# Kernel optimization log

Hardware: AMD Instinct MI355X
Metric: run time of the kernel (lower is better)

## Reference

```python
import jax, jax.numpy as jnp
import numpy as np

H, KV, Dh = 16, 4, 128
ROPE_BASE = 10000.0


def _rope(x, pos):
    # x: (B, nh, T, Dh); pos: (T,)
    inv = 1.0 / (ROPE_BASE ** (jnp.arange(0, Dh, 2, dtype=jnp.float32) / Dh))  # (Dh/2,)
    freqs = pos.astype(jnp.float32)[:, None] * inv[None, :]                    # (T, Dh/2)
    cos = jnp.cos(freqs).astype(x.dtype)[None, None]                           # (1,1,T,Dh/2)
    sin = jnp.sin(freqs).astype(x.dtype)[None, None]
    x1, x2 = x[..., ::2], x[..., 1::2]
    o1 = x1 * cos - x2 * sin
    o2 = x1 * sin + x2 * cos
    return jnp.stack([o1, o2], axis=-1).reshape(x.shape)


def setup_inputs() -> dict:
    key = jax.random.key(0)
    ks = jax.random.split(key, 5)
    B, T, d = 2, 2048, 2048
    s = 1.0 / np.sqrt(d)
    return {
        "x": jax.random.normal(ks[0], (B, T, d), dtype=jnp.float32),
        "Wq": jax.random.normal(ks[1], (d, H * Dh), dtype=jnp.float32) * s,
        "Wk": jax.random.normal(ks[2], (d, KV * Dh), dtype=jnp.float32) * s,
        "Wv": jax.random.normal(ks[3], (d, KV * Dh), dtype=jnp.float32) * s,
        "Wo": jax.random.normal(ks[4], (H * Dh, d), dtype=jnp.float32) * s,
    }


def reference(x, Wq, Wk, Wv, Wo):
    B, T, d = x.shape
    rep = H // KV
    q = (x @ Wq).reshape(B, T, H, Dh).transpose(0, 2, 1, 3)   # (B,H,T,Dh)
    k = (x @ Wk).reshape(B, T, KV, Dh).transpose(0, 2, 1, 3)  # (B,KV,T,Dh)
    v = (x @ Wv).reshape(B, T, KV, Dh).transpose(0, 2, 1, 3)

    pos = jnp.arange(T)
    q = _rope(q, pos)
    k = _rope(k, pos)

    # GQA repeat_kv: (B,KV,T,Dh) -> (B,H,T,Dh), heads repeated consecutively
    k_full = jnp.repeat(k, rep, axis=1)
    v_full = jnp.repeat(v, rep, axis=1)

    scale = 1.0 / np.sqrt(Dh)
    scores = jnp.einsum('bhqd,bhkd->bhqk', q, k_full) * scale  # (B,H,T,T)
    causal = jnp.tril(jnp.ones((T, T), dtype=bool))
    scores = jnp.where(causal[None, None], scores, -jnp.inf)
    attn = jax.nn.softmax(scores, axis=-1)
    out = jnp.einsum('bhqk,bhkd->bhqd', attn, v_full)          # (B,H,T,Dh)
    out = out.transpose(0, 2, 1, 3).reshape(B, T, H * Dh)
    return out @ Wo
```

## Files before the change

### kernel.cpp

```cpp
#include <hip/hip_runtime.h>
#include <stdint.h>

typedef __bf16 bf16;
typedef __bf16 bf16x8 __attribute__((ext_vector_type(8)));
typedef __bf16 bf16x4 __attribute__((ext_vector_type(4)));
typedef float  f32x4  __attribute__((ext_vector_type(4)));

#define T_SEQ  2048
#define NHEAD  16
#define DHEAD  128
#define DMODEL 2048
#define NQKV   3072
#define UNROLL _Pragma("unroll")

__device__ __forceinline__ void gload_lds16(const void* g, void* l) {
  __builtin_amdgcn_global_load_lds(
      (const __attribute__((address_space(1))) uint32_t*)g,
      (__attribute__((address_space(3))) uint32_t*)l, 16, 0, 0);
}

__device__ __forceinline__ void twt_body(const float* __restrict__ W,
                                         bf16* __restrict__ WT, int K, int N,
                                         int bx, int by, float (*t)[65]) {
  int k0 = bx * 64, n0 = by * 64;
  int r4 = threadIdx.x >> 6, c = threadIdx.x & 63;
#pragma unroll
  for (int i = 0; i < 16; i++) {
    int r = i * 4 + r4;
    t[r][c] = W[(size_t)(k0 + r) * N + n0 + c];
  }
  __syncthreads();
#pragma unroll
  for (int i = 0; i < 16; i++) {
    int r = i * 4 + r4;
    WT[(size_t)(n0 + r) * K + k0 + c] = (bf16)t[c][r];
  }
}

__global__ __launch_bounds__(256) void k_prep(const float* __restrict__ x,
                                              const float* __restrict__ Wq,
                                              const float* __restrict__ Wk,
                                              const float* __restrict__ Wv,
                                              const float* __restrict__ Wo,
                                              bf16* __restrict__ xb,
                                              bf16* __restrict__ WT,
                                              bf16* __restrict__ WoT) {
  __shared__ float t[64][65];
  const int blk = blockIdx.x;
  if (blk < 8192) {
    int i = (blk * 256 + threadIdx.x) * 4;
    float4 v = *(const float4*)(x + i);
    bf16x4 o = { (bf16)v.x, (bf16)v.y, (bf16)v.z, (bf16)v.w };
    *(bf16x4*)(xb + i) = o;
  } else if (blk < 9216) {
    int b = blk - 8192;
    twt_body(Wq, WT, 2048, 2048, b & 31, b >> 5, t);
  } else if (blk < 9472) {
    int b = blk - 9216;
    twt_body(Wk, WT + (size_t)2048 * 2048, 2048, 512, b & 31, b >> 5, t);
  } else if (blk < 9728) {
    int b = blk - 9472;
    twt_body(Wv, WT + (size_t)2560 * 2048, 2048, 512, b & 31, b >> 5, t);
  } else {
    int b = blk - 9728;
    twt_body(Wo, WoT, 2048, 2048, b & 31, b >> 5, t);
  }
}

__global__ __launch_bounds__(256) void k_post(bf16* __restrict__ QKV,
                                              bf16* __restrict__ Vtg) {
  __shared__ bf16 t[64][65];
  const int blk = blockIdx.x;
  if (blk < 5120) {
    const float L2B = 0.20762050593046007f;
    int tid = blk * 256 + threadIdx.x;
    int row = tid / 320;
    int c8 = (tid - row * 320) * 8;
    int tt = row & (T_SEQ - 1);
    bf16* p = QKV + (size_t)row * NQKV + c8;
    bf16x8 v = *(const bf16x8*)p;
    int ib = (c8 & 127) >> 1;
    bf16x8 o;
#pragma unroll
    for (int m = 0; m < 4; m++) {
      float inv = exp2f(-(float)(ib + m) * L2B);
      float ang = (float)tt * inv;
      float cs, sn;
      __sincosf(ang, &sn, &cs);
      float x1 = (float)v[2 * m], x2 = (float)v[2 * m + 1];
      o[2 * m]     = (bf16)(x1 * cs - x2 * sn);
      o[2 * m + 1] = (bf16)(x1 * sn + x2 * cs);
    }
    *(bf16x8*)p = o;
  } else {
    int bb = blk - 5120;
    int bx = bb & 31, by = (bb >> 5) & 1, g = bb >> 6;
    const int t0 = bx * 64, d0 = by * 64;
    const int b = g >> 2, kvh = g & 3;
    const bf16* src = QKV + (size_t)b * T_SEQ * NQKV + 2560 + kvh * DHEAD;
    bf16* dst = Vtg + ((size_t)(b * 4 + kvh) * 128 + d0) * T_SEQ + t0;
    const int r4 = threadIdx.x >> 6, c = threadIdx.x & 63;
#pragma unroll
    for (int i = 0; i < 16; i++) {
      int r = i * 4 + r4;
      t[r][c] = src[(size_t)(t0 + r) * NQKV + d0 + c];
    }
    __syncthreads();
#pragma unroll
    for (int i = 0; i < 16; i++) {
      int r = i * 4 + r4;
      dst[(size_t)r * T_SEQ + c] = t[c][r];
    }
  }
}

#define PH(BUF, P, RB, VMW, STAGE) do {                                                   \
    bf16x8 a0k0 = rdA(BUF, 2*(P),     0), a0k1 = rdA(BUF, 2*(P),     1);                  \
    bf16x8 a1k0 = rdA(BUF, 2*(P) + 1, 0), a1k1 = rdA(BUF, 2*(P) + 1, 1);                  \
    if (RB) {                                                                             \
      UNROLL for (int n = 0; n < 4; n++) { b0[n] = rdB(BUF, 0, n); b1[n] = rdB(BUF, 1, n); } \
    }                                                                                     \
    STAGE                                                                                 \
    __builtin_amdgcn_sched_barrier(0);                                                    \
    __builtin_amdgcn_s_barrier();                                                         \
    asm volatile("s_waitcnt lgkmcnt(0)" ::: "memory");                                    \
    __builtin_amdgcn_sched_barrier(0);                                                    \
    __builtin_amdgcn_s_setprio(1);                                                        \
    UNROLL for (int n = 0; n < 4; n++) {                                                  \
      acc[2*(P)][n]   = __builtin_amdgcn_mfma_f32_16x16x32_bf16(a0k0, b0[n], acc[2*(P)][n], 0, 0, 0);     \
      acc[2*(P)][n]   = __builtin_amdgcn_mfma_f32_16x16x32_bf16(a0k1, b1[n], acc[2*(P)][n], 0, 0, 0);     \
      acc[2*(P)+1][n] = __builtin_amdgcn_mfma_f32_16x16x32_bf16(a1k0, b0[n], acc[2*(P)+1][n], 0, 0, 0);   \
      acc[2*(P)+1][n] = __builtin_amdgcn_mfma_f32_16x16x32_bf16(a1k1, b1[n], acc[2*(P)+1][n], 0, 0, 0);   \
    }                                                                                     \
    __builtin_amdgcn_s_setprio(0);                                                        \
    if (VMW) { asm volatile("s_waitcnt vmcnt(4)" ::: "memory"); }                         \
    __builtin_amdgcn_sched_barrier(0);                                                    \
    __builtin_amdgcn_s_barrier();                                                         \
  } while (0)

template<bool F32OUT>
__global__ __launch_bounds__(512) void k_gemm2(const bf16* __restrict__ A,
                                               const bf16* __restrict__ BT,
                                               void* __restrict__ C,
                                               int M, int N, int K) {
  __shared__ __align__(16) bf16 L[2][2][2][8192];
  const int nwg = gridDim.x * gridDim.y;
  const int orig = blockIdx.y * gridDim.x + blockIdx.x;
  const int tile = (orig & 7) * (nwg >> 3) + (orig >> 3);
  const int m0 = (tile % gridDim.x) * 256, n0 = (tile / gridDim.x) * 256;
  const int tid = threadIdx.x;
  const int lane = tid & 63, w = tid >> 6;
  const int wr = w >> 2, wc = w & 3;
  const int l15 = lane & 15, lg = lane >> 4;
  const int srow = tid >> 3;
  const int scol = ((tid & 7) ^ (srow & 7)) * 8;
  const int NKT = K >> 6;

  f32x4 acc[8][4] = {};
  bf16x8 b0[4], b1[4];

  auto stA = [&](int buf, int half, int kt) {
    const bf16* g = A + (size_t)(m0 + half * 128 + srow) * K + kt * 64 + scol;
    bf16* lb = &L[buf][0][half][w * 512];
    gload_lds16(g, lb);
    gload_lds16(g + (size_t)64 * K, lb + 4096);
  };
  auto stB = [&](int buf, int half, int kt) {
    const bf16* g = BT + (size_t)(n0 + half * 128 + srow) * K + kt * 64 + scol;
    bf16* lb = &L[buf][1][half][w * 512];
    gload_lds16(g, lb);
    gload_lds16(g + (size_t)64 * K, lb + 4096);
  };
  auto rdA = [&](int buf, int fr, int kk) -> bf16x8 {
    int r = fr * 16 + l15;
    return *(const bf16x8*)((const char*)&L[buf][0][wr][0] + r * 128 +
                            (((kk * 4 + lg) ^ (r & 7)) << 4));
  };
  auto rdB = [&](int buf, int kk, int n) -> bf16x8 {
    int rr = wc * 64 + n * 16 + l15;
    return *(const bf16x8*)((const char*)&L[buf][1][rr >> 7][0] + (rr & 127) * 128 +
                            (((kk * 4 + lg) ^ (rr & 7)) << 4));
  };

  stA(0, 0, 0); stA(0, 1, 0);
  stB(0, 0, 0); stB(0, 1, 0);
  stB(1, 0, 1); stB(1, 1, 1);
  asm volatile("s_waitcnt vmcnt(4)" ::: "memory");
  __builtin_amdgcn_sched_barrier(0);
  __builtin_amdgcn_s_barrier();

  for (int it = 0; it < (NKT >> 1); ++it) {
    const int t1 = 2 * it + 1;
    const int t2 = (t1 + 1 < NKT) ? t1 + 1 : NKT - 1;
    const int t3 = (t1 + 2 < NKT) ? t1 + 2 : NKT - 1;
    PH(0, 0, 1, 0, stA(1, 0, t1););
    PH(0, 1, 0, 0, stA(1, 1, t1););
    PH(0, 2, 0, 0, stB(0, 0, t2););
    PH(0, 3, 0, 1, stB(0, 1, t2););
    PH(1, 0, 1, 0, stA(0, 0, t2););
    PH(1, 1, 0, 0, stA(0, 1, t2););
    PH(1, 2, 0, 0, stB(1, 0, t3););
    PH(1, 3, 0, 1, stB(1, 1, t3););
  }

  const int r0 = m0 + wr * 128 + lg * 4;
  const int c0 = n0 + wc * 64 + l15;
  UNROLL for (int m = 0; m < 8; m++)
    UNROLL for (int n = 0; n < 4; n++)
      UNROLL for (int i = 0; i < 4; i++) {
        size_t idx = (size_t)(r0 + m * 16 + i) * N + (c0 + n * 16);
        if (F32OUT) ((float*)C)[idx] = acc[m][n][i];
        else        ((bf16*)C)[idx]  = (bf16)acc[m][n][i];
      }
}

#define COMPUTE2(kt, cur) do {                                                            \
    f32x4 sA_[4] = {}, sB_[4] = {};                                                       \
    const char* ks_ = (const char*)Ks[cur];                                               \
    __builtin_amdgcn_s_setprio(1);                                                        \
    UNROLL for (int kk = 0; kk < 4; kk++)                                                 \
      UNROLL for (int n = 0; n < 4; n++) {                                                \
        int row_ = n * 16 + l15;                                                          \
        int cb_ = (kk * 64 + lg * 16) ^ ((row_ & 7) << 4);                                \
        bf16x8 kf_ = *(const bf16x8*)(ks_ + row_ * 256 + cb_);                            \
        sA_[n] = __builtin_amdgcn_mfma_f32_16x16x32_bf16(kf_, qA[kk], sA_[n], 0, 0, 0);   \
        sB_[n] = __builtin_amdgcn_mfma_f32_16x16x32_bf16(kf_, qB[kk], sB_[n], 0, 0, 0);   \
      }                                                                                   \
    __builtin_amdgcn_s_setprio(0);                                                        \
    float vmA_ = -1e30f, vmB_ = -1e30f;                                                   \
    if ((kt) == qt) {                                                                     \
      UNROLL for (int n = 0; n < 4; n++)                                                  \
        UNROLL for (int i = 0; i < 4; i++) {                                              \
          if ((kt) * 64 + n * 16 + lg * 4 + i > qglob) {                                  \
            sA_[n][i] = -1e30f; sB_[n][i] = -1e30f;                                       \
          }                                                                               \
          vmA_ = fmaxf(vmA_, sA_[n][i]);                                                  \
          vmB_ = fmaxf(vmB_, sB_[n][i]);                                                  \
        }                                                                                 \
    } else {                                                                              \
      UNROLL for (int n = 0; n < 4; n++)                                                  \
        UNROLL for (int i = 0; i < 4; i++) {                                              \
          vmA_ = fmaxf(vmA_, sA_[n][i]);                                                  \
          vmB_ = fmaxf(vmB_, sB_[n][i]);                                                  \
        }                                                                                 \
    }                                                                                     \
    vmA_ = fmaxf(vmA_, __shfl_xor(vmA_, 16));                                             \
    vmA_ = fmaxf(vmA_, __shfl_xor(vmA_, 32));                                             \
    vmB_ = fmaxf(vmB_, __shfl_xor(vmB_, 16));                                             \
    vmB_ = fmaxf(vmB_, __shfl_xor(vmB_, 32));                                             \
    if (!__all((vmA_ <= mA + 8.0f) && (vmB_ <= mB + 8.0f))) {                             \
      float mnA_ = fmaxf(mA, vmA_), mnB_ = fmaxf(mB, vmB_);                               \
      float alA_ = __builtin_amdgcn_exp2f(mA - mnA_);                                     \
      float alB_ = __builtin_amdgcn_exp2f(mB - mnB_);                                     \
      mA = mnA_; mB = mnB_;                                                               \
      lA *= alA_; lB *= alB_;                                                             \
      UNROLL for (int i = 0; i < 4; i++) {                                                \
        int src_ = (lane & 48) + ((lane >> 2) & 12) + i;                                  \
        float aA_ = __shfl(alA_, src_);                                                   \
        float aB_ = __shfl(alB_, src_);                                                   \
        UNROLL for (int n = 0; n < 8; n++) { oA[n][i] *= aA_; oB[n][i] *= aB_; }          \
      }                                                                                   \
    }                                                                                     \
    bf16x8 paA0_, paA1_, paB0_, paB1_;                                                    \
    {                                                                                     \
      float rs_ = 0.f;                                                                    \
      UNROLL for (int n = 0; n < 4; n++) {                                                \
        bf16x4 pk_;                                                                       \
        UNROLL for (int i = 0; i < 4; i++) {                                              \
          float pv_ = __builtin_amdgcn_exp2f(sA_[n][i] - mA);                             \
          rs_ += pv_;                                                                     \
          pk_[i] = (bf16)pv_;                                                             \
        }                                                                                 \
        *(bf16x4*)(&Ps[w][l15][n * 16 + lg * 4]) = pk_;                                   \
      }                                                                                   \
      rs_ += __shfl_xor(rs_, 16);                                                         \
      rs_ += __shfl_xor(rs_, 32);                                                         \
      lA += rs_;                                                                          \
      paA0_ = *(const bf16x8*)(&Ps[w][l15][lg * 8]);                                      \
      paA1_ = *(const bf16x8*)(&Ps[w][l15][32 + lg * 8]);                                 \
    }                                                                                     \
    {                                                                                     \
      float rs_ = 0.f;                                                                    \
      UNROLL for (int n = 0; n < 4; n++) {                                                \
        bf16x4 pk_;                                                                       \
        UNROLL for (int i = 0; i < 4; i++) {                                              \
          float pv_ = __builtin_amdgcn_exp2f(sB_[n][i] - mB);                             \
          rs_ += pv_;                                                                     \
          pk_[i] = (bf16)pv_;                                                             \
        }                                                                                 \
        *(bf16x4*)(&Ps[w][l15][n * 16 + lg * 4]) = pk_;                                   \
      }                                                                                   \
      rs_ += __shfl_xor(rs_, 16);                                                         \
      rs_ += __shfl_xor(rs_, 32);                                                         \
      lB += rs_;                                                                          \
      paB0_ = *(const bf16x8*)(&Ps[w][l15][lg * 8]);                                      \
      paB1_ = *(const bf16x8*)(&Ps[w][l15][32 + lg * 8]);                                 \
    }                                                                                     \
    const char* vs_ = (const char*)Vs[cur];                                               \
    __builtin_amdgcn_s_setprio(1);                                                        \
    UNROLL for (int n = 0; n < 8; n++) {                                                  \
      int d_ = n * 16 + l15;                                                              \
      bf16x8 vf0_ = *(const bf16x8*)(vs_ + d_ * 128 + (((lg) ^ (d_ & 7)) << 4));          \
      oA[n] = __builtin_amdgcn_mfma_f32_16x16x32_bf16(paA0_, vf0_, oA[n], 0, 0, 0);       \
      oB[n] = __builtin_amdgcn_mfma_f32_16x16x32_bf16(paB0_, vf0_, oB[n], 0, 0, 0);       \
      bf16x8 vf1_ = *(const bf16x8*)(vs_ + d_ * 128 + (((4 + lg) ^ (d_ & 7)) << 4));      \
      oA[n] = __builtin_amdgcn_mfma_f32_16x16x32_bf16(paA1_, vf1_, oA[n], 0, 0, 0);       \
      oB[n] = __builtin_amdgcn_mfma_f32_16x16x32_bf16(paB1_, vf1_, oB[n], 0, 0, 0);       \
    }                                                                                     \
    __builtin_amdgcn_s_setprio(0);                                                        \
  } while (0)

__global__ __launch_bounds__(256) void k_flash(const bf16* __restrict__ QKV,
                                               const bf16* __restrict__ Vtg,
                                               bf16* __restrict__ AO) {
  __shared__ __align__(16) bf16 Ks[2][64 * 128];
  __shared__ __align__(16) bf16 Vs[2][128 * 64];
  __shared__ __align__(16) bf16 Ps[4][16][72];
  const int orig = blockIdx.y * 32 + blockIdx.x;
  const int fin  = ((orig & 7) << 6) | (orig >> 3);
  const int bhp  = fin >> 5;
  const int qt   = 31 - (fin & 31);
  const int b = bhp >> 3, kvh = (bhp >> 1) & 3, hp = bhp & 1;
  const int h0 = kvh * 4 + hp * 2, h1 = h0 + 1;
  const int tid = threadIdx.x, lane = tid & 63, w = tid >> 6;
  const int l15 = lane & 15, lg = lane >> 4;
  const int qglob = qt * 64 + w * 16 + l15;
  const float qs = 0.12753102f;

  bf16x8 qA[4], qB[4];
  {
    const size_t qoA = (size_t)(b * T_SEQ + qt * 64 + w * 16 + l15) * NQKV + h0 * DHEAD;
    const size_t qoB = (size_t)(b * T_SEQ + qt * 64 + w * 16 + l15) * NQKV + h1 * DHEAD;
    UNROLL for (int kk = 0; kk < 4; kk++) {
      bf16x8 a = *(const bf16x8*)(QKV + qoA + kk * 32 + lg * 8);
      bf16x8 bb = *(const bf16x8*)(QKV + qoB + kk * 32 + lg * 8);
      UNROLL for (int j = 0; j < 8; j++) {
        a[j] = (bf16)((float)a[j] * qs);
        bb[j] = (bf16)((float)bb[j] * qs);
      }
      qA[kk] = a; qB[kk] = bb;
    }
  }

  f32x4 oA[8] = {}, oB[8] = {};
  float mA = -1e30f, mB = -1e30f, lA = 0.f, lB = 0.f;

  const bf16* Kbase = QKV + (size_t)b * T_SEQ * NQKV + DMODEL + kvh * DHEAD;
  const bf16* Vbase = Vtg + (size_t)(b * 4 + kvh) * 128 * T_SEQ;

  auto issueK = [&](int buf, int kt) {
    UNROLL for (int i = 0; i < 4; i++) {
      int row = w * 16 + i * 4 + lg;
      int col = (l15 ^ (row & 7)) * 8;
      gload_lds16(Kbase + (size_t)(kt * 64 + row) * NQKV + col,
                  Ks[buf] + (w * 4 + i) * 512);
    }
  };
  auto issueV = [&](int buf, int kt) {
    UNROLL for (int i = 0; i < 4; i++) {
      int d = (w * 4 + i) * 8 + (lane >> 3);
      int u = lane & 7;
      gload_lds16(Vbase + (size_t)d * T_SEQ + kt * 64 + ((u ^ (d & 7)) * 8),
                  Vs[buf] + (w * 4 + i) * 512);
    }
  };

  issueK(0, 0);
  issueV(0, 0);
  __syncthreads();

  const int NT = qt + 1;
  for (int kt = 0; kt < NT; kt++) {
    const int cur = kt & 1, nxt = cur ^ 1;
    if (kt + 1 < NT) { issueK(nxt, kt + 1); issueV(nxt, kt + 1); }
    COMPUTE2(kt, cur);
    __syncthreads();
  }

  {
    const size_t ob0 = (size_t)(b * T_SEQ + qt * 64 + w * 16 + lg * 4) * DMODEL + h0 * DHEAD + l15;
    const size_t ob1 = (size_t)(b * T_SEQ + qt * 64 + w * 16 + lg * 4) * DMODEL + h1 * DHEAD + l15;
    UNROLL for (int i = 0; i < 4; i++) {
      int src = (lane & 48) + ((lane >> 2) & 12) + i;
      float invA = 1.0f / __shfl(lA, src);
      float invB = 1.0f / __shfl(lB, src);
      UNROLL for (int n = 0; n < 8; n++) {
        AO[ob0 + (size_t)i * DMODEL + n * 16] = (bf16)(oA[n][i] * invA);
        AO[ob1 + (size_t)i * DMODEL + n * 16] = (bf16)(oB[n][i] * invB);
      }
    }
  }
}

extern "C" void kernel_launch(void* const* d_in, const int* in_sizes, int n_in,
                              void* d_out, int out_size, void* d_ws, size_t ws_size,
                              hipStream_t stream) {
  const float* x  = (const float*)d_in[0];
  const float* Wq = (const float*)d_in[1];
  const float* Wk = (const float*)d_in[2];
  const float* Wv = (const float*)d_in[3];
  const float* Wo = (const float*)d_in[4];
  char* ws = (char*)d_ws;
  bf16* xb  = (bf16*)ws;
  bf16* WT  = (bf16*)(ws + 16777216ull);
  bf16* WoT = (bf16*)(ws + 16777216ull + 12582912ull);
  bf16* QKV = (bf16*)(ws + 16777216ull + 12582912ull + 8388608ull);
  bf16* AO  = (bf16*)(ws + 16777216ull + 12582912ull + 8388608ull + 25165824ull);
  bf16* Vtg = WT;
  float* out = (float*)d_out;

  k_prep<<<10752, 256, 0, stream>>>(x, Wq, Wk, Wv, Wo, xb, WT, WoT);
  k_gemm2<false><<<dim3(16, 12), 512, 0, stream>>>(xb, WT, QKV, 4096, 3072, 2048);
  k_post<<<5632, 256, 0, stream>>>(QKV, Vtg);
  k_flash<<<dim3(32, 16), 256, 0, stream>>>(QKV, Vtg, AO);
  k_gemm2<true><<<dim3(16, 8), 512, 0, stream>>>(AO, WoT, out, 4096, 2048, 2048);
}
```

Baseline: 219.1 us.

## Pair complementary causal query tiles per block to balance flash-attention work

Each flash-attention block now handles one head and two query tiles, p and 31-p, instead of two heads sharing one query tile. Every block therefore does about the same number of KV iterations, which removes the tail imbalance from causal masking. The A half of the compute is skipped once the loop passes its diagonal. The cost is K/V reuse across two heads of the same KV group: each block now serves only one head, and the per-iteration code branches between two macro instantiations.

```diff
diff --git a/kernel.cpp b/kernel.cpp
--- a/kernel.cpp
+++ b/kernel.cpp
@@ -214,7 +214,7 @@
       }
 }
 
-#define COMPUTE2(kt, cur) do {                                                            \
+#define COMP(kt, cur, DOA) do {                                                           \
     f32x4 sA_[4] = {}, sB_[4] = {};                                                       \
     const char* ks_ = (const char*)Ks[cur];                                               \
     __builtin_amdgcn_s_setprio(1);                                                        \
@@ -223,46 +223,58 @@
         int row_ = n * 16 + l15;                                                          \
         int cb_ = (kk * 64 + lg * 16) ^ ((row_ & 7) << 4);                                \
         bf16x8 kf_ = *(const bf16x8*)(ks_ + row_ * 256 + cb_);                            \
-        sA_[n] = __builtin_amdgcn_mfma_f32_16x16x32_bf16(kf_, qA[kk], sA_[n], 0, 0, 0);   \
+        if (DOA) sA_[n] = __builtin_amdgcn_mfma_f32_16x16x32_bf16(kf_, qA[kk], sA_[n], 0, 0, 0); \
         sB_[n] = __builtin_amdgcn_mfma_f32_16x16x32_bf16(kf_, qB[kk], sB_[n], 0, 0, 0);   \
       }                                                                                   \
     __builtin_amdgcn_s_setprio(0);                                                        \
     float vmA_ = -1e30f, vmB_ = -1e30f;                                                   \
-    if ((kt) == qt) {                                                                     \
+    if ((DOA && (kt) == qtA) || (kt) == qtB) {                                            \
       UNROLL for (int n = 0; n < 4; n++)                                                  \
         UNROLL for (int i = 0; i < 4; i++) {                                              \
-          if ((kt) * 64 + n * 16 + lg * 4 + i > qglob) {                                  \
-            sA_[n][i] = -1e30f; sB_[n][i] = -1e30f;                                       \
+          int kvg_ = (kt) * 64 + n * 16 + lg * 4 + i;                                     \
+          if (DOA) {                                                                      \
+            if ((kt) == qtA && kvg_ > qglobA) sA_[n][i] = -1e30f;                         \
+            vmA_ = fmaxf(vmA_, sA_[n][i]);                                                \
           }                                                                               \
-          vmA_ = fmaxf(vmA_, sA_[n][i]);                                                  \
+          if ((kt) == qtB && kvg_ > qglobB) sB_[n][i] = -1e30f;                           \
           vmB_ = fmaxf(vmB_, sB_[n][i]);                                                  \
         }                                                                                 \
     } else {                                                                              \
       UNROLL for (int n = 0; n < 4; n++)                                                  \
         UNROLL for (int i = 0; i < 4; i++) {                                              \
-          vmA_ = fmaxf(vmA_, sA_[n][i]);                                                  \
+          if (DOA) vmA_ = fmaxf(vmA_, sA_[n][i]);                                         \
           vmB_ = fmaxf(vmB_, sB_[n][i]);                                                  \
         }                                                                                 \
     }                                                                                     \
-    vmA_ = fmaxf(vmA_, __shfl_xor(vmA_, 16));                                             \
-    vmA_ = fmaxf(vmA_, __shfl_xor(vmA_, 32));                                             \
     vmB_ = fmaxf(vmB_, __shfl_xor(vmB_, 16));                                             \
     vmB_ = fmaxf(vmB_, __shfl_xor(vmB_, 32));                                             \
-    if (!__all((vmA_ <= mA + 8.0f) && (vmB_ <= mB + 8.0f))) {                             \
-      float mnA_ = fmaxf(mA, vmA_), mnB_ = fmaxf(mB, vmB_);                               \
-      float alA_ = __builtin_amdgcn_exp2f(mA - mnA_);                                     \
+    if (DOA) {                                                                            \
+      vmA_ = fmaxf(vmA_, __shfl_xor(vmA_, 16));                                           \
+      vmA_ = fmaxf(vmA_, __shfl_xor(vmA_, 32));                                           \
+    }                                                                                     \
+    bool ok_ = (vmB_ <= mB + 8.0f) && (!(DOA) || (vmA_ <= mA + 8.0f));                    \
+    if (!__all(ok_)) {                                                                    \
+      float mnB_ = fmaxf(mB, vmB_);                                                       \
       float alB_ = __builtin_amdgcn_exp2f(mB - mnB_);                                     \
-      mA = mnA_; mB = mnB_;                                                               \
-      lA *= alA_; lB *= alB_;                                                             \
+      mB = mnB_; lB *= alB_;                                                              \
+      float alA_ = 0.f;                                                                   \
+      if (DOA) {                                                                          \
+        float mnA_ = fmaxf(mA, vmA_);                                                     \
+        alA_ = __builtin_amdgcn_exp2f(mA - mnA_);                                         \
+        mA = mnA_; lA *= alA_;                                                            \
+      }                                                                                   \
       UNROLL for (int i = 0; i < 4; i++) {                                                \
         int src_ = (lane & 48) + ((lane >> 2) & 12) + i;                                  \
-        float aA_ = __shfl(alA_, src_);                                                   \
         float aB_ = __shfl(alB_, src_);                                                   \
-        UNROLL for (int n = 0; n < 8; n++) { oA[n][i] *= aA_; oB[n][i] *= aB_; }          \
+        float aA_ = (DOA) ? __shfl(alA_, src_) : 0.f;                                     \
+        UNROLL for (int n = 0; n < 8; n++) {                                              \
+          oB[n][i] *= aB_;                                                                \
+          if (DOA) oA[n][i] *= aA_;                                                       \
+        }                                                                                 \
       }                                                                                   \
     }                                                                                     \
     bf16x8 paA0_, paA1_, paB0_, paB1_;                                                    \
-    {                                                                                     \
+    if (DOA) {                                                                            \
       float rs_ = 0.f;                                                                    \
       UNROLL for (int n = 0; n < 4; n++) {                                                \
         bf16x4 pk_;                                                                       \
@@ -301,10 +313,10 @@
     UNROLL for (int n = 0; n < 8; n++) {                                                  \
       int d_ = n * 16 + l15;                                                              \
       bf16x8 vf0_ = *(const bf16x8*)(vs_ + d_ * 128 + (((lg) ^ (d_ & 7)) << 4));          \
-      oA[n] = __builtin_amdgcn_mfma_f32_16x16x32_bf16(paA0_, vf0_, oA[n], 0, 0, 0);       \
+      if (DOA) oA[n] = __builtin_amdgcn_mfma_f32_16x16x32_bf16(paA0_, vf0_, oA[n], 0, 0, 0); \
       oB[n] = __builtin_amdgcn_mfma_f32_16x16x32_bf16(paB0_, vf0_, oB[n], 0, 0, 0);       \
       bf16x8 vf1_ = *(const bf16x8*)(vs_ + d_ * 128 + (((4 + lg) ^ (d_ & 7)) << 4));      \
-      oA[n] = __builtin_amdgcn_mfma_f32_16x16x32_bf16(paA1_, vf1_, oA[n], 0, 0, 0);       \
+      if (DOA) oA[n] = __builtin_amdgcn_mfma_f32_16x16x32_bf16(paA1_, vf1_, oA[n], 0, 0, 0); \
       oB[n] = __builtin_amdgcn_mfma_f32_16x16x32_bf16(paB1_, vf1_, oB[n], 0, 0, 0);       \
     }                                                                                     \
     __builtin_amdgcn_s_setprio(0);                                                        \
@@ -316,21 +328,22 @@
   __shared__ __align__(16) bf16 Ks[2][64 * 128];
   __shared__ __align__(16) bf16 Vs[2][128 * 64];
   __shared__ __align__(16) bf16 Ps[4][16][72];
-  const int orig = blockIdx.y * 32 + blockIdx.x;
-  const int fin  = ((orig & 7) << 6) | (orig >> 3);
-  const int bhp  = fin >> 5;
-  const int qt   = 31 - (fin & 31);
-  const int b = bhp >> 3, kvh = (bhp >> 1) & 3, hp = bhp & 1;
-  const int h0 = kvh * 4 + hp * 2, h1 = h0 + 1;
+  const int orig = blockIdx.y * 16 + blockIdx.x;
+  const int xcd = orig & 7, idx = orig >> 3;
+  const int b = xcd >> 2, kvh = xcd & 3;
+  const int h = kvh * 4 + (idx >> 4);
+  const int p = idx & 15;
+  const int qtA = p, qtB = 31 - p;
   const int tid = threadIdx.x, lane = tid & 63, w = tid >> 6;
   const int l15 = lane & 15, lg = lane >> 4;
-  const int qglob = qt * 64 + w * 16 + l15;
+  const int qglobA = qtA * 64 + w * 16 + l15;
+  const int qglobB = qtB * 64 + w * 16 + l15;
   const float qs = 0.12753102f;
 
   bf16x8 qA[4], qB[4];
   {
-    const size_t qoA = (size_t)(b * T_SEQ + qt * 64 + w * 16 + l15) * NQKV + h0 * DHEAD;
-    const size_t qoB = (size_t)(b * T_SEQ + qt * 64 + w * 16 + l15) * NQKV + h1 * DHEAD;
+    const size_t qoA = (size_t)(b * T_SEQ + qtA * 64 + w * 16 + l15) * NQKV + h * DHEAD;
+    const size_t qoB = (size_t)(b * T_SEQ + qtB * 64 + w * 16 + l15) * NQKV + h * DHEAD;
     UNROLL for (int kk = 0; kk < 4; kk++) {
       bf16x8 a = *(const bf16x8*)(QKV + qoA + kk * 32 + lg * 8);
       bf16x8 bb = *(const bf16x8*)(QKV + qoB + kk * 32 + lg * 8);
@@ -369,17 +382,18 @@
   issueV(0, 0);
   __syncthreads();
 
-  const int NT = qt + 1;
+  const int NT = qtB + 1;
   for (int kt = 0; kt < NT; kt++) {
     const int cur = kt & 1, nxt = cur ^ 1;
     if (kt + 1 < NT) { issueK(nxt, kt + 1); issueV(nxt, kt + 1); }
-    COMPUTE2(kt, cur);
+    if (kt <= qtA) COMP(kt, cur, 1);
+    else           COMP(kt, cur, 0);
     __syncthreads();
   }
 
   {
-    const size_t ob0 = (size_t)(b * T_SEQ + qt * 64 + w * 16 + lg * 4) * DMODEL + h0 * DHEAD + l15;
-    const size_t ob1 = (size_t)(b * T_SEQ + qt * 64 + w * 16 + lg * 4) * DMODEL + h1 * DHEAD + l15;
+    const size_t ob0 = (size_t)(b * T_SEQ + qtA * 64 + w * 16 + lg * 4) * DMODEL + h * DHEAD + l15;
+    const size_t ob1 = (size_t)(b * T_SEQ + qtB * 64 + w * 16 + lg * 4) * DMODEL + h * DHEAD + l15;
     UNROLL for (int i = 0; i < 4; i++) {
       int src = (lane & 48) + ((lane >> 2) & 12) + i;
       float invA = 1.0f / __shfl(lA, src);
@@ -412,6 +426,6 @@
   k_prep<<<10752, 256, 0, stream>>>(x, Wq, Wk, Wv, Wo, xb, WT, WoT);
   k_gemm2<false><<<dim3(16, 12), 512, 0, stream>>>(xb, WT, QKV, 4096, 3072, 2048);
   k_post<<<5632, 256, 0, stream>>>(QKV, Vtg);
-  k_flash<<<dim3(32, 16), 256, 0, stream>>>(QKV, Vtg, AO);
+  k_flash<<<dim3(16, 32), 256, 0, stream>>>(QKV, Vtg, AO);
   k_gemm2<true><<<dim3(16, 8), 512, 0, stream>>>(AO, WoT, out, 4096, 2048, 2048);
 }
```

New measurement: 242.1 us. +10.5%, slower.

## Single-buffer K/V tiles in flash attention with split-phase prefetch

Applied to the files above, without the earlier changes.

Replaces the double-buffered K and V shared-memory tiles with single buffers. The next K tile is now prefetched right after the QK^T MFMAs, behind a barrier, and the next V tile right after the PV MFMAs, behind a second barrier. The main aim is to roughly halve LDS use per block so more blocks can be resident per CU. The cost is an extra barrier per iteration and less time for each tile load to land before it is used.

```diff
diff --git a/kernel.cpp b/kernel.cpp
--- a/kernel.cpp
+++ b/kernel.cpp
@@ -214,9 +214,9 @@
       }
 }
 
-#define COMPUTE2(kt, cur) do {                                                            \
+#define COMPUTE2(kt) do {                                                                 \
     f32x4 sA_[4] = {}, sB_[4] = {};                                                       \
-    const char* ks_ = (const char*)Ks[cur];                                               \
+    const char* ks_ = (const char*)Ks;                                                    \
     __builtin_amdgcn_s_setprio(1);                                                        \
     UNROLL for (int kk = 0; kk < 4; kk++)                                                 \
       UNROLL for (int n = 0; n < 4; n++) {                                                \
@@ -227,6 +227,8 @@
         sB_[n] = __builtin_amdgcn_mfma_f32_16x16x32_bf16(kf_, qB[kk], sB_[n], 0, 0, 0);   \
       }                                                                                   \
     __builtin_amdgcn_s_setprio(0);                                                        \
+    __syncthreads();                               \
+    if ((kt) + 1 < NT) issueK((kt) + 1);                \
     float vmA_ = -1e30f, vmB_ = -1e30f;                                                   \
     if ((kt) == qt) {                                                                     \
       UNROLL for (int n = 0; n < 4; n++)                                                  \
@@ -296,7 +298,7 @@
       paB0_ = *(const bf16x8*)(&Ps[w][l15][lg * 8]);                                      \
       paB1_ = *(const bf16x8*)(&Ps[w][l15][32 + lg * 8]);                                 \
     }                                                                                     \
-    const char* vs_ = (const char*)Vs[cur];                                               \
+    const char* vs_ = (const char*)Vs;                                                    \
     __builtin_amdgcn_s_setprio(1);                                                        \
     UNROLL for (int n = 0; n < 8; n++) {                                                  \
       int d_ = n * 16 + l15;                                                              \
@@ -308,13 +310,15 @@
       oB[n] = __builtin_amdgcn_mfma_f32_16x16x32_bf16(paB1_, vf1_, oB[n], 0, 0, 0);       \
     }                                                                                     \
     __builtin_amdgcn_s_setprio(0);                                                        \
+    __syncthreads();                             \
+    if ((kt) + 1 < NT) issueV((kt) + 1);              \
   } while (0)
 
 __global__ __launch_bounds__(256) void k_flash(const bf16* __restrict__ QKV,
                                                const bf16* __restrict__ Vtg,
                                                bf16* __restrict__ AO) {
-  __shared__ __align__(16) bf16 Ks[2][64 * 128];
-  __shared__ __align__(16) bf16 Vs[2][128 * 64];
+  __shared__ __align__(16) bf16 Ks[64 * 128];
+  __shared__ __align__(16) bf16 Vs[128 * 64];
   __shared__ __align__(16) bf16 Ps[4][16][72];
   const int orig = blockIdx.y * 32 + blockIdx.x;
   const int fin  = ((orig & 7) << 6) | (orig >> 3);
@@ -348,33 +352,30 @@
   const bf16* Kbase = QKV + (size_t)b * T_SEQ * NQKV + DMODEL + kvh * DHEAD;
   const bf16* Vbase = Vtg + (size_t)(b * 4 + kvh) * 128 * T_SEQ;
 
-  auto issueK = [&](int buf, int kt) {
+  auto issueK = [&](int kt) {
     UNROLL for (int i = 0; i < 4; i++) {
       int row = w * 16 + i * 4 + lg;
       int col = (l15 ^ (row & 7)) * 8;
       gload_lds16(Kbase + (size_t)(kt * 64 + row) * NQKV + col,
-                  Ks[buf] + (w * 4 + i) * 512);
-    }
-  };
-  auto issueV = [&](int buf, int kt) {
+                  Ks + (w * 4 + i) * 512);
+    }
+  };
+  auto issueV = [&](int kt) {
     UNROLL for (int i = 0; i < 4; i++) {
       int d = (w * 4 + i) * 8 + (lane >> 3);
       int u = lane & 7;
       gload_lds16(Vbase + (size_t)d * T_SEQ + kt * 64 + ((u ^ (d & 7)) * 8),
-                  Vs[buf] + (w * 4 + i) * 512);
-    }
-  };
-
-  issueK(0, 0);
-  issueV(0, 0);
+                  Vs + (w * 4 + i) * 512);
+    }
+  };
+
+  issueK(0);
+  issueV(0);
   __syncthreads();
 
   const int NT = qt + 1;
   for (int kt = 0; kt < NT; kt++) {
-    const int cur = kt & 1, nxt = cur ^ 1;
-    if (kt + 1 < NT) { issueK(nxt, kt + 1); issueV(nxt, kt + 1); }
-    COMPUTE2(kt, cur);
-    __syncthreads();
+    COMPUTE2(kt);
   }
 
   {
```

Measured after the change: 205.7 us. 1.06x faster.
